# Optimization experiments

Measured on AMD Instinct MI355X. Metric: run time of the kernel, lower is better.

The kernel has to match this reference:

```python
import jax, jax.numpy as jnp
import numpy as np


def _hconv(x, src, eid, W, b, num_nodes, num_edges, att=None, hattr=None):
    """PyG HypergraphConv (heads=1, concat=True), optional node-mode attention.
    src: node index per incidence; eid: hyperedge index per incidence."""
    F = W.shape[0]
    xw = x @ W.T                                  # [N, F]
    alpha = None
    if att is not None:
        he = hattr @ W.T                          # [num_edges, F]
        # (cat([x_i, e_j]) * att).sum(-1) == x_i@att[:F] + e_j@att[F:]
        a = (xw @ att[:F])[src] + (he @ att[F:])[eid]   # [nnz]
        a = jnp.where(a > 0, a, 0.2 * a)          # leaky_relu(0.2)
        # node-mode softmax: normalize over incidences sharing the same hyperedge
        amax = jax.ops.segment_max(a, eid, num_segments=num_edges)
        ex = jnp.exp(a - amax[eid])
        denom = jax.ops.segment_sum(ex, eid, num_segments=num_edges)
        alpha = ex / denom[eid]
    ones = jnp.ones(src.shape[0], xw.dtype)
    Dn = jax.ops.segment_sum(ones, src, num_segments=num_nodes)   # node degree
    Dinv = jnp.where(Dn > 0, 1.0 / Dn, 0.0)
    Bn = jax.ops.segment_sum(ones, eid, num_segments=num_edges)   # edge degree
    Binv = jnp.where(Bn > 0, 1.0 / Bn, 0.0)
    # node -> hyperedge
    msg = Binv[eid][:, None] * xw[src]            # [nnz, F]
    if alpha is not None:
        msg = alpha[:, None] * msg
    efeat = jax.ops.segment_sum(msg, eid, num_segments=num_edges)
    # hyperedge -> node
    msg2 = Dinv[src][:, None] * efeat[eid]
    if alpha is not None:
        msg2 = alpha[:, None] * msg2
    return jax.ops.segment_sum(msg2, src, num_segments=num_nodes) + b


def setup_inputs() -> dict:
    key = jax.random.key(0)
    ks = jax.random.split(key, 13)
    D, M, Vc, Vm, F = 512, 1024, 2000, 2000, 64
    return {
        "c_it": jax.random.randint(ks[0], (D,), 0, Vc),
        "medicine_it": jax.random.randint(ks[1], (M,), 0, Vm),
        "c_embeddings": jax.random.normal(ks[2], (Vc, F), jnp.float32),
        "m_embeddings": jax.random.normal(ks[3], (Vm, F), jnp.float32),
        "pe0": jax.random.normal(ks[4], (Vc, F), jnp.float32),
        "pe1": jax.random.normal(ks[5], (Vm, F), jnp.float32),
        "conv_w": jax.random.normal(ks[6], (F, F), jnp.float32) / np.sqrt(F),
        "conv_b": jax.random.normal(ks[7], (F,), jnp.float32) * 0.02,
        "gat_w": jax.random.normal(ks[8], (F, F), jnp.float32) / np.sqrt(F),
        "gat_b": jax.random.normal(ks[9], (F,), jnp.float32) * 0.02,
        "gat_att": jax.random.normal(ks[10], (2 * F,), jnp.float32) / np.sqrt(2 * F),
        "hyperedge_attr": jax.random.normal(ks[11], (D, F), jnp.float32),
        "lin_w": jax.random.normal(ks[12], (F, 2 * F), jnp.float32) / np.sqrt(2 * F),
    }


def reference(c_it, medicine_it, c_embeddings, m_embeddings, pe0, pe1,
              conv_w, conv_b, gat_w, gat_b, gat_att, hyperedge_attr, lin_w):
    D = c_it.shape[0]
    M = medicine_it.shape[0]
    # single-hyperedge graphs over diseases and over meds
    dia_feat = _hconv(c_embeddings[c_it], jnp.arange(D), jnp.zeros(D, jnp.int32),
                      conv_w, conv_b, D, 1)
    med_feat = _hconv(m_embeddings[medicine_it], jnp.arange(M), jnp.zeros(M, jnp.int32),
                      conv_w, conv_b, M, 1)
    # dual hypergraph: hyperedge e = {disease e} U {all meds}
    comb = jnp.concatenate([c_embeddings[c_it], m_embeddings[medicine_it]], axis=0)  # [D+M, F]
    src = jnp.concatenate([jnp.arange(D)[:, None],
                           jnp.broadcast_to(jnp.arange(D, D + M), (D, M))],
                          axis=1).reshape(-1)                    # [D*(M+1)]
    eid = jnp.repeat(jnp.arange(D), M + 1)                       # [D*(M+1)]
    dm_feat = _hconv(comb, src, eid, gat_w, gat_b, D + M, D,
                     att=gat_att, hattr=hyperedge_attr)
    rep = jnp.concatenate([jnp.concatenate([dm_feat[:D], dia_feat], axis=1),
                           jnp.concatenate([dm_feat[D:], med_feat], axis=1)], axis=0)
    rep = rep @ lin_w.T                                          # [D+M, 64]
    # resi_output: vectorized sum over index loops
    i1 = (pe0[c_it].sum(0) + rep[:D].sum(0)).reshape(1, 1, -1)
    i2 = (pe1[medicine_it].sum(0) + rep[D:].sum(0)).reshape(1, 1, -1)
    return (i1, i2)
```

## Files before the change

kernel.cpp:

```cpp
#include <hip/hip_runtime.h>
#include <hip/hip_bf16.h>

#define D_N 512
#define M_N 1024
#define F_N 64
#define L2E 1.442695041f

__device__ __forceinline__ float wred_sum(float p) {
#pragma unroll
    for (int off = 32; off > 0; off >>= 1) p += __shfl_xor(p, off, 64);
    return p;
}

__device__ __forceinline__ float proj_col(const float* __restrict__ gw,
                                          const float* __restrict__ att,
                                          int lane) {
    float acc = 0.f;
#pragma unroll
    for (int k = 0; k < 64; ++k)
        acc += att[k] * gw[k * 64 + lane];
    return acc;
}

__global__ __launch_bounds__(512) void kprep(
    const int* __restrict__ c_it, const int* __restrict__ m_it,
    const float* __restrict__ c_emb, const float* __restrict__ m_emb,
    const float* __restrict__ pe0, const float* __restrict__ pe1,
    const float* __restrict__ gat_w, const float* __restrict__ gat_att,
    const float* __restrict__ hattr,
    float* __restrict__ umed, float* __restrict__ uc, float* __restrict__ v,
    float* __restrict__ pp)
{
    __shared__ __align__(16) float qs[64];
    __shared__ float redA[8][64], redB[8][64];
    const int b = blockIdx.x, tid = threadIdx.x;
    const int w = tid >> 6, lane = tid & 63;

    if (b < 96) {
        if (w == 0) qs[lane] = proj_col(gat_w, gat_att, lane);
        __syncthreads();
        const int* idx; const float* ta; const float* tb;
        float* dout; int base_r, oA, oB;
        if (b < 32) { idx = c_it; ta = pe0; tb = c_emb; dout = uc;
                      base_r = b * 16; oA = b; oB = 32 + b; }
        else { int g2 = b - 32; idx = m_it; ta = pe1; tb = m_emb; dout = umed;
               base_r = g2 * 16; oA = 64 + g2; oB = 128 + g2; }
        const int r0 = base_r + w * 2;
        float a = 0.f, bb = 0.f;
#pragma unroll
        for (int j = 0; j < 2; ++j) {
            const int row = r0 + j;
            const int r = idx[row];
            float av = ta[(size_t)r * F_N + lane];
            float bv = tb[(size_t)r * F_N + lane];
            a += av; bb += bv;
            float d = wred_sum(bv * qs[lane]);
            if (lane == 0) dout[row] = L2E * d;
        }
        redA[w][lane] = a; redB[w][lane] = bb;
        __syncthreads();
        if (w == 0) {
            float sa = 0.f, sbv = 0.f;
#pragma unroll
            for (int i = 0; i < 8; ++i) { sa += redA[i][lane]; sbv += redB[i][lane]; }
            pp[oA * 64 + lane] = sa;
            pp[oB * 64 + lane] = sbv;
        }
    } else {
        if (w == 0) qs[lane] = proj_col(gat_w, gat_att + 64, lane);
        __syncthreads();
        const int r0 = (b - 96) * 16 + w * 2;
#pragma unroll
        for (int j = 0; j < 2; ++j) {
            const int row = r0 + j;
            float hv = hattr[(size_t)row * F_N + lane];
            float d = wred_sum(hv * qs[lane]);
            if (lane == 0) v[row] = L2E * d;
        }
    }
}

__global__ __launch_bounds__(512) void kedge(
    const int* __restrict__ c_it, const float* __restrict__ c_emb,
    const float* __restrict__ umed_g, const float* __restrict__ uc,
    const float* __restrict__ v,
    float* __restrict__ c1f, float* __restrict__ c2f,
    float* __restrict__ e1dp, float* __restrict__ e2dp)
{
    __shared__ float umed[M_N];
    __shared__ float redA[8][64], redB[8][64];
    const int b = blockIdx.x, tid = threadIdx.x;
    const int w = tid >> 6, lane = tid & 63;

    umed[tid] = umed_g[tid];
    umed[tid + 512] = umed_g[tid + 512];
    __syncthreads();

    const int e = b * 8 + w;
    const float ve = v[e];
    float s = 0.f;
#pragma unroll
    for (int i = 0; i < 16; ++i) {
        float a = umed[i * 64 + lane] + ve;
        a = fmaxf(a, 0.2f * a);
        s += exp2f(a);
    }
    s = wred_sum(s);
    float asf = uc[e] + ve; asf = fmaxf(asf, 0.2f * asf);
    const float exs = exp2f(asf);
    const float denom = s + exs;
    const float asel = exs / denom;
    const float rd = 1.f / (denom * (float)(M_N + 1));
    if (lane == 0) {
        c1f[e] = asel * rd;
        c2f[e] = (1.f - asel) * rd;
    }
    const float w1a = asel * rd * exs;
    const float w2a = (1.f - asel) * rd * exs;
    const float xe = c_emb[(size_t)c_it[e] * F_N + lane];
    redA[w][lane] = w1a * xe;
    redB[w][lane] = w2a * xe;
    __syncthreads();
    if (w == 0) {
        float sa = 0.f, sbv = 0.f;
#pragma unroll
        for (int i = 0; i < 8; ++i) { sa += redA[i][lane]; sbv += redB[i][lane]; }
        e1dp[b * 64 + lane] = sa;
        e2dp[b * 64 + lane] = sbv;
    }
}

__global__ __launch_bounds__(512) void kmed(
    const int* __restrict__ m_it, const float* __restrict__ m_emb,
    const float* __restrict__ umed_g, const float* __restrict__ v,
    const float* __restrict__ c1f, const float* __restrict__ c2f,
    float* __restrict__ e1p, float* __restrict__ e2p)
{
    __shared__ float sV[D_N], sC1[D_N], sC2[D_N];
    __shared__ float sUm[16], sG1[16], sG2[16];
    __shared__ float redA[8][64], redB[8][64];
    const int b = blockIdx.x, tid = threadIdx.x;
    const int w = tid >> 6, lane = tid & 63;
    const int m_base = b * 16;

    sV[tid] = v[tid]; sC1[tid] = c1f[tid]; sC2[tid] = c2f[tid];
    if (tid < 16) sUm[tid] = umed_g[m_base + tid];
    __syncthreads();

    {
        const int mi = tid >> 5, l32 = tid & 31;
        const float um = sUm[mi];
        float gA = 0.f, gB = 0.f;
#pragma unroll 4
        for (int i = 0; i < 16; ++i) {
            int e = l32 + i * 32;
            float a = um + sV[e];
            a = fmaxf(a, 0.2f * a);
            float ex = exp2f(a);
            gA += sC1[e] * ex;
            gB += sC2[e] * ex;
        }
#pragma unroll
        for (int off = 1; off < 32; off <<= 1) {
            gA += __shfl_xor(gA, off, 64);
            gB += __shfl_xor(gB, off, 64);
        }
        if (l32 == 0) { sG1[mi] = gA; sG2[mi] = gB; }
    }
    __syncthreads();
    float a1 = 0.f, a2 = 0.f;
#pragma unroll
    for (int j = 0; j < 2; ++j) {
        int ml = w * 2 + j;
        float x = m_emb[(size_t)m_it[m_base + ml] * F_N + lane];
        a1 += sG1[ml] * x;
        a2 += sG2[ml] * x;
    }
    redA[w][lane] = a1; redB[w][lane] = a2;
    __syncthreads();
    if (w == 0) {
        float sa = 0.f, sbv = 0.f;
#pragma unroll
        for (int i = 0; i < 8; ++i) { sa += redA[i][lane]; sbv += redB[i][lane]; }
        e1p[b * 64 + lane] = sa;
        e2p[b * 64 + lane] = sbv;
    }
}

__global__ __launch_bounds__(512) void kfin(
    const float* __restrict__ conv_w, const float* __restrict__ conv_b,
    const float* __restrict__ gat_w, const float* __restrict__ gat_b,
    const float* __restrict__ lin_w,
    const float* __restrict__ pp,
    const float* __restrict__ e1p, const float* __restrict__ e2p,
    const float* __restrict__ e1dp, const float* __restrict__ e2dp,
    float* __restrict__ out)
{
    __shared__ float pA[8][64], pB[8][64];
    __shared__ float sE1[64], sE2[64], sP0[64], sP1[64], sMC[64], sMM[64];
    __shared__ float sS1[64], sS2[64];
    __shared__ float sRepD[128], sRepM[128];
    __shared__ float sWt[64 * 65];
    __shared__ float sLt[128 * 65];
    const int tid = threadIdx.x, w = tid >> 6, lane = tid & 63;

    {
        float a = 0.f, bb = 0.f;
        switch (w) {
        case 0:
#pragma unroll
            for (int i = 0; i < 64; ++i) a += e1p[i * 64 + lane];
            break;
        case 1:
#pragma unroll
            for (int i = 0; i < 64; ++i) a += e1dp[i * 64 + lane];
            break;
        case 2:
#pragma unroll
            for (int i = 0; i < 64; ++i) a += e2p[i * 64 + lane];
            break;
        case 3:
#pragma unroll
            for (int i = 0; i < 64; ++i) a += e2dp[i * 64 + lane];
            break;
        case 4:
#pragma unroll
            for (int i = 0; i < 32; ++i) { a += pp[i * 64 + lane]; bb += pp[(32 + i) * 64 + lane]; }
            break;
        case 5:
#pragma unroll
            for (int i = 0; i < 64; ++i) a += pp[(64 + i) * 64 + lane];
            break;
        default:
#pragma unroll
            for (int i = 0; i < 64; ++i) a += pp[(128 + i) * 64 + lane];
            break;
        }
        pA[w][lane] = a; pB[w][lane] = bb;
    }
    for (int i = tid; i < 4096; i += 512)
        sWt[(i & 63) * 65 + (i >> 6)] = gat_w[i];
    for (int i = tid; i < 8192; i += 512) {
        int k = i >> 7, j = i & 127;
        sLt[j * 65 + k] = lin_w[i];
    }
    __syncthreads();
    if (w == 0) {
        sE1[lane] = pA[0][lane] + pA[1][lane];
        sE2[lane] = pA[2][lane] + pA[3][lane];
        sP0[lane] = pA[4][lane];
        sMC[lane] = pB[4][lane] * (1.f / (float)D_N);
        sP1[lane] = pA[5][lane];
        sMM[lane] = pA[6][lane] * (1.f / (float)M_N);
    }
    __syncthreads();
    if (tid < 64) {
        float s1 = 0.f, s2 = 0.f;
#pragma unroll 8
        for (int j = 0; j < 64; ++j) {
            s1 += sE1[j] * sWt[j * 65 + lane];
            s2 += sE2[j] * sWt[j * 65 + lane];
        }
        sS1[lane] = s1;
        sS2[lane] = s2 * (1.f / (float)D_N);
    }
    __syncthreads();
    for (int i = tid; i < 4096; i += 512)
        sWt[(i & 63) * 65 + (i >> 6)] = conv_w[i];
    __syncthreads();
    if (tid < 64) {
        float dia = conv_b[lane], med = conv_b[lane];
#pragma unroll 8
        for (int j = 0; j < 64; ++j) {
            dia += sMC[j] * sWt[j * 65 + lane];
            med += sMM[j] * sWt[j * 65 + lane];
        }
        sRepD[lane]      = sS1[lane] + (float)D_N * gat_b[lane];
        sRepD[64 + lane] = (float)D_N * dia;
        sRepM[lane]      = sS2[lane] + (float)M_N * gat_b[lane];
        sRepM[64 + lane] = (float)M_N * med;
    }
    __syncthreads();
    if (tid < 64) {
        float o1 = sP0[lane], o2 = sP1[lane];
#pragma unroll 8
        for (int j = 0; j < 128; ++j) {
            o1 += sRepD[j] * sLt[j * 65 + lane];
            o2 += sRepM[j] * sLt[j * 65 + lane];
        }
        out[lane] = o1;
        out[64 + lane] = o2;
    }
}

extern "C" void kernel_launch(void* const* d_in, const int* in_sizes, int n_in,
                              void* d_out, int out_size, void* d_ws, size_t ws_size,
                              hipStream_t stream) {
    const int*   c_it    = (const int*)d_in[0];
    const int*   m_it    = (const int*)d_in[1];
    const float* c_emb   = (const float*)d_in[2];
    const float* m_emb   = (const float*)d_in[3];
    const float* pe0     = (const float*)d_in[4];
    const float* pe1     = (const float*)d_in[5];
    const float* conv_w  = (const float*)d_in[6];
    const float* conv_b  = (const float*)d_in[7];
    const float* gat_w   = (const float*)d_in[8];
    const float* gat_b   = (const float*)d_in[9];
    const float* gat_att = (const float*)d_in[10];
    const float* hattr   = (const float*)d_in[11];
    const float* lin_w   = (const float*)d_in[12];
    float* out = (float*)d_out;

    float* ws   = (float*)d_ws;
    float* umed = ws;
    float* uc   = umed + M_N;
    float* v    = uc + D_N;
    float* c1f  = v + D_N;
    float* c2f  = c1f + D_N;
    float* pp   = c2f + D_N;
    float* e1p  = pp + 192 * 64;
    float* e2p  = e1p + 64 * 64;
    float* e1dp = e2p + 64 * 64;
    float* e2dp = e1dp + 64 * 64;

    kprep<<<128, 512, 0, stream>>>(c_it, m_it, c_emb, m_emb, pe0, pe1,
                                   gat_w, gat_att, hattr, umed, uc, v, pp);
    kedge<<<64, 512, 0, stream>>>(c_it, c_emb, umed, uc, v,
                                  c1f, c2f, e1dp, e2dp);
    kmed<<<64, 512, 0, stream>>>(m_it, m_emb, umed, v, c1f, c2f, e1p, e2p);
    kfin<<<1, 512, 0, stream>>>(conv_w, conv_b, gat_w, gat_b, lin_w,
                                pp, e1p, e2p, e1dp, e2dp, out);
}
```

Measured before the change: 23.78 us.

## Spread final reductions across waves and hoist gathers earlier in kernels

In kfin, the partial-sum reductions are now spread across all 8 waves instead of one wave per buffer. conv_w is staged into its own shared tile up front, which removes a reload and a barrier. The two small matvecs run on separate waves in parallel. In kprep, kedge and kmed, global gathers are issued before the dependent compute so their latency overlaps the exp/reduction work, and kedge reads umed directly from global instead of staging it in LDS. This adds shared memory in kfin, which may lower occupancy, but that kernel is a single block.

```diff
diff --git a/kernel.cpp b/kernel.cpp
--- a/kernel.cpp
+++ b/kernel.cpp
@@ -46,18 +46,15 @@
         else { int g2 = b - 32; idx = m_it; ta = pe1; tb = m_emb; dout = umed;
                base_r = g2 * 16; oA = 64 + g2; oB = 128 + g2; }
         const int r0 = base_r + w * 2;
-        float a = 0.f, bb = 0.f;
-#pragma unroll
-        for (int j = 0; j < 2; ++j) {
-            const int row = r0 + j;
-            const int r = idx[row];
-            float av = ta[(size_t)r * F_N + lane];
-            float bv = tb[(size_t)r * F_N + lane];
-            a += av; bb += bv;
-            float d = wred_sum(bv * qs[lane]);
-            if (lane == 0) dout[row] = L2E * d;
-        }
-        redA[w][lane] = a; redB[w][lane] = bb;
+        const int ra = idx[r0], rb = idx[r0 + 1];
+        const float ta0 = ta[(size_t)ra * F_N + lane];
+        const float tb0 = tb[(size_t)ra * F_N + lane];
+        const float ta1 = ta[(size_t)rb * F_N + lane];
+        const float tb1 = tb[(size_t)rb * F_N + lane];
+        float d0 = wred_sum(tb0 * qs[lane]);
+        float d1 = wred_sum(tb1 * qs[lane]);
+        if (lane == 0) { dout[r0] = L2E * d0; dout[r0 + 1] = L2E * d1; }
+        redA[w][lane] = ta0 + ta1; redB[w][lane] = tb0 + tb1;
         __syncthreads();
         if (w == 0) {
             float sa = 0.f, sbv = 0.f;
@@ -70,13 +67,11 @@
         if (w == 0) qs[lane] = proj_col(gat_w, gat_att + 64, lane);
         __syncthreads();
         const int r0 = (b - 96) * 16 + w * 2;
-#pragma unroll
-        for (int j = 0; j < 2; ++j) {
-            const int row = r0 + j;
-            float hv = hattr[(size_t)row * F_N + lane];
-            float d = wred_sum(hv * qs[lane]);
-            if (lane == 0) v[row] = L2E * d;
-        }
+        const float h0 = hattr[(size_t)r0 * F_N + lane];
+        const float h1 = hattr[(size_t)(r0 + 1) * F_N + lane];
+        float d0 = wred_sum(h0 * qs[lane]);
+        float d1 = wred_sum(h1 * qs[lane]);
+        if (lane == 0) { v[r0] = L2E * d0; v[r0 + 1] = L2E * d1; }
     }
 }
 
@@ -87,26 +82,24 @@
     float* __restrict__ c1f, float* __restrict__ c2f,
     float* __restrict__ e1dp, float* __restrict__ e2dp)
 {
-    __shared__ float umed[M_N];
     __shared__ float redA[8][64], redB[8][64];
     const int b = blockIdx.x, tid = threadIdx.x;
     const int w = tid >> 6, lane = tid & 63;
 
-    umed[tid] = umed_g[tid];
-    umed[tid + 512] = umed_g[tid + 512];
-    __syncthreads();
-
     const int e = b * 8 + w;
     const float ve = v[e];
+    const float uce = uc[e];
+    const float xe = c_emb[(size_t)c_it[e] * F_N + lane];
+
     float s = 0.f;
 #pragma unroll
     for (int i = 0; i < 16; ++i) {
-        float a = umed[i * 64 + lane] + ve;
+        float a = umed_g[i * 64 + lane] + ve;
         a = fmaxf(a, 0.2f * a);
         s += exp2f(a);
     }
     s = wred_sum(s);
-    float asf = uc[e] + ve; asf = fmaxf(asf, 0.2f * asf);
+    float asf = uce + ve; asf = fmaxf(asf, 0.2f * asf);
     const float exs = exp2f(asf);
     const float denom = s + exs;
     const float asel = exs / denom;
@@ -115,11 +108,8 @@
         c1f[e] = asel * rd;
         c2f[e] = (1.f - asel) * rd;
     }
-    const float w1a = asel * rd * exs;
-    const float w2a = (1.f - asel) * rd * exs;
-    const float xe = c_emb[(size_t)c_it[e] * F_N + lane];
-    redA[w][lane] = w1a * xe;
-    redB[w][lane] = w2a * xe;
+    redA[w][lane] = (asel * rd * exs) * xe;
+    redB[w][lane] = ((1.f - asel) * rd * exs) * xe;
     __syncthreads();
     if (w == 0) {
         float sa = 0.f, sbv = 0.f;
@@ -143,6 +133,10 @@
     const int w = tid >> 6, lane = tid & 63;
     const int m_base = b * 16;
 
+    const int ml0 = w * 2, ml1 = w * 2 + 1;
+    const float x0 = m_emb[(size_t)m_it[m_base + ml0] * F_N + lane];
+    const float x1 = m_emb[(size_t)m_it[m_base + ml1] * F_N + lane];
+
     sV[tid] = v[tid]; sC1[tid] = c1f[tid]; sC2[tid] = c2f[tid];
     if (tid < 16) sUm[tid] = umed_g[m_base + tid];
     __syncthreads();
@@ -168,15 +162,8 @@
         if (l32 == 0) { sG1[mi] = gA; sG2[mi] = gB; }
     }
     __syncthreads();
-    float a1 = 0.f, a2 = 0.f;
-#pragma unroll
-    for (int j = 0; j < 2; ++j) {
-        int ml = w * 2 + j;
-        float x = m_emb[(size_t)m_it[m_base + ml] * F_N + lane];
-        a1 += sG1[ml] * x;
-        a2 += sG2[ml] * x;
-    }
-    redA[w][lane] = a1; redB[w][lane] = a2;
+    redA[w][lane] = sG1[ml0] * x0 + sG1[ml1] * x1;
+    redB[w][lane] = sG2[ml0] * x0 + sG2[ml1] * x1;
     __syncthreads();
     if (w == 0) {
         float sa = 0.f, sbv = 0.f;
@@ -196,65 +183,83 @@
     const float* __restrict__ e1dp, const float* __restrict__ e2dp,
     float* __restrict__ out)
 {
-    __shared__ float pA[8][64], pB[8][64];
+    __shared__ float pA8[8][8][64];
     __shared__ float sE1[64], sE2[64], sP0[64], sP1[64], sMC[64], sMM[64];
-    __shared__ float sS1[64], sS2[64];
+    __shared__ float sS1[64], sS2[64], sDia[64], sMed[64];
     __shared__ float sRepD[128], sRepM[128];
     __shared__ float sWt[64 * 65];
+    __shared__ float sCt[64 * 65];
     __shared__ float sLt[128 * 65];
     const int tid = threadIdx.x, w = tid >> 6, lane = tid & 63;
 
     {
-        float a = 0.f, bb = 0.f;
-        switch (w) {
-        case 0:
-#pragma unroll
-            for (int i = 0; i < 64; ++i) a += e1p[i * 64 + lane];
-            break;
-        case 1:
-#pragma unroll
-            for (int i = 0; i < 64; ++i) a += e1dp[i * 64 + lane];
-            break;
-        case 2:
-#pragma unroll
-            for (int i = 0; i < 64; ++i) a += e2p[i * 64 + lane];
-            break;
-        case 3:
-#pragma unroll
-            for (int i = 0; i < 64; ++i) a += e2dp[i * 64 + lane];
-            break;
-        case 4:
-#pragma unroll
-            for (int i = 0; i < 32; ++i) { a += pp[i * 64 + lane]; bb += pp[(32 + i) * 64 + lane]; }
-            break;
-        case 5:
-#pragma unroll
-            for (int i = 0; i < 64; ++i) a += pp[(64 + i) * 64 + lane];
-            break;
-        default:
-#pragma unroll
-            for (int i = 0; i < 64; ++i) a += pp[(128 + i) * 64 + lane];
-            break;
-        }
-        pA[w][lane] = a; pB[w][lane] = bb;
-    }
-    for (int i = tid; i < 4096; i += 512)
+        float a0 = 0.f, a1 = 0.f, a2 = 0.f, a3 = 0.f;
+        float a4 = 0.f, a5 = 0.f, a6 = 0.f, a7 = 0.f;
+#pragma unroll
+        for (int k = 0; k < 8; ++k) {
+            const int i = w + 8 * k;
+            a0 += e1p[i * 64 + lane];
+            a1 += e1dp[i * 64 + lane];
+            a2 += e2p[i * 64 + lane];
+            a3 += e2dp[i * 64 + lane];
+            a6 += pp[(64 + i) * 64 + lane];
+            a7 += pp[(128 + i) * 64 + lane];
+        }
+#pragma unroll
+        for (int k = 0; k < 4; ++k) {
+            const int i = w + 8 * k;
+            a4 += pp[i * 64 + lane];
+            a5 += pp[(32 + i) * 64 + lane];
+        }
+        pA8[0][w][lane] = a0; pA8[1][w][lane] = a1;
+        pA8[2][w][lane] = a2; pA8[3][w][lane] = a3;
+        pA8[4][w][lane] = a4; pA8[5][w][lane] = a5;
+        pA8[6][w][lane] = a6; pA8[7][w][lane] = a7;
+    }
+    for (int i = tid; i < 4096; i += 512) {
         sWt[(i & 63) * 65 + (i >> 6)] = gat_w[i];
+        sCt[(i & 63) * 65 + (i >> 6)] = conv_w[i];
+    }
     for (int i = tid; i < 8192; i += 512) {
         int k = i >> 7, j = i & 127;
         sLt[j * 65 + k] = lin_w[i];
     }
     __syncthreads();
-    if (w == 0) {
-        sE1[lane] = pA[0][lane] + pA[1][lane];
-        sE2[lane] = pA[2][lane] + pA[3][lane];
-        sP0[lane] = pA[4][lane];
-        sMC[lane] = pB[4][lane] * (1.f / (float)D_N);
-        sP1[lane] = pA[5][lane];
-        sMM[lane] = pA[6][lane] * (1.f / (float)M_N);
-    }
-    __syncthreads();
-    if (tid < 64) {
+
+    if (w == 0) {
+        float a = 0.f;
+#pragma unroll
+        for (int j = 0; j < 8; ++j) a += pA8[0][j][lane] + pA8[1][j][lane];
+        sE1[lane] = a;
+    } else if (w == 1) {
+        float a = 0.f;
+#pragma unroll
+        for (int j = 0; j < 8; ++j) a += pA8[2][j][lane] + pA8[3][j][lane];
+        sE2[lane] = a;
+    } else if (w == 2) {
+        float a = 0.f;
+#pragma unroll
+        for (int j = 0; j < 8; ++j) a += pA8[4][j][lane];
+        sP0[lane] = a;
+    } else if (w == 3) {
+        float a = 0.f;
+#pragma unroll
+        for (int j = 0; j < 8; ++j) a += pA8[5][j][lane];
+        sMC[lane] = a * (1.f / (float)D_N);
+    } else if (w == 4) {
+        float a = 0.f;
+#pragma unroll
+        for (int j = 0; j < 8; ++j) a += pA8[6][j][lane];
+        sP1[lane] = a;
+    } else if (w == 5) {
+        float a = 0.f;
+#pragma unroll
+        for (int j = 0; j < 8; ++j) a += pA8[7][j][lane];
+        sMM[lane] = a * (1.f / (float)M_N);
+    }
+    __syncthreads();
+
+    if (w == 0) {
         float s1 = 0.f, s2 = 0.f;
 #pragma unroll 8
         for (int j = 0; j < 64; ++j) {
@@ -263,25 +268,22 @@
         }
         sS1[lane] = s1;
         sS2[lane] = s2 * (1.f / (float)D_N);
-    }
-    __syncthreads();
-    for (int i = tid; i < 4096; i += 512)
-        sWt[(i & 63) * 65 + (i >> 6)] = conv_w[i];
-    __syncthreads();
-    if (tid < 64) {
+    } else if (w == 1) {
         float dia = conv_b[lane], med = conv_b[lane];
 #pragma unroll 8
         for (int j = 0; j < 64; ++j) {
-            dia += sMC[j] * sWt[j * 65 + lane];
-            med += sMM[j] * sWt[j * 65 + lane];
-        }
+            dia += sMC[j] * sCt[j * 65 + lane];
+            med += sMM[j] * sCt[j * 65 + lane];
+        }
+        sDia[lane] = dia; sMed[lane] = med;
+    }
+    __syncthreads();
+
+    if (w == 0) {
         sRepD[lane]      = sS1[lane] + (float)D_N * gat_b[lane];
-        sRepD[64 + lane] = (float)D_N * dia;
+        sRepD[64 + lane] = (float)D_N * sDia[lane];
         sRepM[lane]      = sS2[lane] + (float)M_N * gat_b[lane];
-        sRepM[64 + lane] = (float)M_N * med;
-    }
-    __syncthreads();
-    if (tid < 64) {
+        sRepM[64 + lane] = (float)M_N * sMed[lane];
         float o1 = sP0[lane], o2 = sP1[lane];
 #pragma unroll 8
         for (int j = 0; j < 128; ++j) {
```

Measured after the change: 22.67 us. 4.7% less time.
